# Kernel tuning notes

Hardware: AMD Instinct MI355X
Metric: run time of the kernel (lower is better)

Reference implementation:

```python
import jax, jax.numpy as jnp
import numpy as np

D_MODEL = 1024
NUM_HEADS = 16
D_K = D_MODEL // NUM_HEADS


def setup_inputs() -> dict:
    key = jax.random.key(0)
    ks = jax.random.split(key, 5)
    sd = np.sqrt(2.0 / (D_MODEL + D_MODEL))
    x = jax.random.normal(ks[0], (2, 2048, D_MODEL), dtype=jnp.float32)
    # weights stored as [out_features, in_features] like torch Linear
    w_q = jax.random.normal(ks[1], (D_MODEL, D_MODEL), dtype=jnp.float32) * (sd * sd)
    w_k = jax.random.normal(ks[2], (D_MODEL, D_MODEL), dtype=jnp.float32) * (sd * sd)
    w_v = jax.random.normal(ks[3], (D_MODEL, D_MODEL), dtype=jnp.float32) * (sd * sd)
    w_o = jax.random.normal(ks[4], (D_MODEL, D_MODEL), dtype=jnp.float32) * (sd * sd)
    return {"x": x, "w_q": w_q, "w_k": w_k, "w_v": w_v, "w_o": w_o}


def reference(x, w_q, w_k, w_v, w_o):
    B, S, D = x.shape
    H, Dk = NUM_HEADS, D_K
    # projections: x @ W.T
    q = (x @ w_q.T).reshape(B, S, H, Dk).transpose(0, 2, 1, 3)  # [B,H,S,Dk]
    k = (x @ w_k.T).reshape(B, S, H, Dk).transpose(0, 2, 1, 3)
    v = (x @ w_v.T).reshape(B, S, H, Dk).transpose(0, 2, 1, 3)
    scale = 1.0 / np.sqrt(Dk).astype(np.float32)
    scores = jnp.einsum('bhqd,bhkd->bhqk', q, k) * scale  # [B,H,S,S]
    causal = jnp.tril(jnp.ones((S, S), dtype=bool))
    scores = jnp.where(causal, scores, -jnp.inf)
    weights = jax.nn.softmax(scores, axis=-1)
    attn = jnp.einsum('bhqk,bhkd->bhqd', weights, v)  # [B,H,S,Dk]
    attn = attn.transpose(0, 2, 1, 3).reshape(B, S, D)
    return attn @ w_o.T
```

## Files before the change

kernel.cpp:

```cpp
#include <hip/hip_runtime.h>

typedef __attribute__((ext_vector_type(8))) short short8;
typedef __attribute__((ext_vector_type(4))) float f32x4;
typedef __attribute__((ext_vector_type(16))) float f32x16;
typedef __attribute__((ext_vector_type(2))) unsigned int u32x2;

#define DM 1024
#define SL 2048
#define NH 16
#define DKH 64
#define NB 2

__device__ __forceinline__ unsigned short f2bf(float f) {
    union { float f; unsigned int u; } a; a.f = f;
    unsigned int r = a.u + 0x7FFFu + ((a.u >> 16) & 1u);
    return (unsigned short)(r >> 16);
}

__device__ __forceinline__ void gl_lds16(const void* g, void* l) {
    __builtin_amdgcn_global_load_lds(
        (__attribute__((address_space(1))) void*)(g),
        (__attribute__((address_space(3))) void*)(l), 16, 0, 0);
}

__device__ __forceinline__ unsigned int cvtpk_bf16(float lo, float hi) {
    unsigned int r;
    asm("v_cvt_pk_bf16_f32 %0, %1, %2" : "=v"(r) : "v"(lo), "v"(hi));
    return r;
}

__device__ __forceinline__ void pl32swap(unsigned int &a, unsigned int &b) {
    u32x2 r = __builtin_amdgcn_permlane32_swap(a, b, false, false);
    a = r[0]; b = r[1];
}
__device__ __forceinline__ void pl32swapf(float &a, float &b) {
    unsigned int ua = __float_as_uint(a), ub = __float_as_uint(b);
    pl32swap(ua, ub);
    a = __uint_as_float(ua); b = __uint_as_float(ub);
}

__global__ __launch_bounds__(256) void convert_kernel(
    const float* __restrict__ x,  const float* __restrict__ wq,
    const float* __restrict__ wk, const float* __restrict__ wv,
    const float* __restrict__ wo,
    unsigned short* __restrict__ xb,  unsigned short* __restrict__ wqb,
    unsigned short* __restrict__ wkb, unsigned short* __restrict__ wvb,
    unsigned short* __restrict__ wob)
{
    const int NX = NB * SL * DM;
    const int NW = DM * DM;
    int t4 = (blockIdx.x * 256 + threadIdx.x) * 4;
    const float* src; unsigned short* dst; int off; float scale = 1.0f;
    if (t4 < NX)              { src = x;  dst = xb;  off = t4; }
    else if (t4 < NX + NW)    { src = wq; dst = wqb; off = t4 - NX; scale = 0.125f * 1.44269504088896f; }
    else if (t4 < NX + 2*NW)  { src = wk; dst = wkb; off = t4 - NX - NW; }
    else if (t4 < NX + 3*NW)  { src = wv; dst = wvb; off = t4 - NX - 2*NW; }
    else                      { src = wo; dst = wob; off = t4 - NX - 3*NW; }
    float4 v = *(const float4*)(src + off);
    unsigned long long p =
        (unsigned long long)f2bf(v.x * scale)
      | ((unsigned long long)f2bf(v.y * scale) << 16)
      | ((unsigned long long)f2bf(v.z * scale) << 32)
      | ((unsigned long long)f2bf(v.w * scale) << 48);
    *(unsigned long long*)(dst + off) = p;
}

template<int MODE>
__global__ __launch_bounds__(256) void gemm_bt(
    const unsigned short* __restrict__ A,
    const unsigned short* __restrict__ Bw,
    unsigned short* __restrict__ oq, unsigned short* __restrict__ ok,
    unsigned short* __restrict__ ov, float* __restrict__ of)
{
    __shared__ __align__(16) unsigned short As[128 * 64];
    __shared__ __align__(16) unsigned short Bs[128 * 64];
    const int tid  = threadIdx.x;
    const int lane = tid & 63;
    const int wave = tid >> 6;
    const int wm = (wave >> 1) * 64, wn = (wave & 1) * 64;
    const int bx = blockIdx.x, by = blockIdx.y;
    const int c    = lane & 15;
    const int kg16 = (lane >> 4) * 16;
    const int swz  = (c & 7) << 4;

    f32x4 acc[4][4];
    #pragma unroll
    for (int i = 0; i < 4; i++)
        #pragma unroll
        for (int j = 0; j < 4; j++) acc[i][j] = (f32x4){0.f, 0.f, 0.f, 0.f};

    const char* Ab = (const char*)A  + by * 128 * (DM * 2);
    const char* Bb = (const char*)Bw + bx * 128 * (DM * 2);

    for (int k0 = 0; k0 < DM; k0 += 64) {
        #pragma unroll
        for (int i = 0; i < 4; i++) {
            int o  = i * 4096 + tid * 16;
            int r  = o >> 7;
            int cb = o & 127;
            int src = r * (DM * 2) + k0 * 2 + (cb ^ ((r & 7) << 4));
            gl_lds16(Ab + src, (char*)As + o);
            gl_lds16(Bb + src, (char*)Bs + o);
        }
        __syncthreads();
        #pragma unroll
        for (int kk = 0; kk < 2; kk++) {
            short8 a[4], bfr[4];
            #pragma unroll
            for (int mi = 0; mi < 4; mi++)
                a[mi] = *(const short8*)((const char*)As
                        + (wm + mi * 16 + c) * 128 + ((kk * 64 + kg16) ^ swz));
            #pragma unroll
            for (int ni = 0; ni < 4; ni++)
                bfr[ni] = *(const short8*)((const char*)Bs
                        + (wn + ni * 16 + c) * 128 + ((kk * 64 + kg16) ^ swz));
            #pragma unroll
            for (int mi = 0; mi < 4; mi++)
                #pragma unroll
                for (int ni = 0; ni < 4; ni++)
                    acc[mi][ni] = __builtin_amdgcn_mfma_f32_16x16x32_bf16(
                        a[mi], bfr[ni], acc[mi][ni], 0, 0, 0);
        }
        __syncthreads();
    }

    const int r4 = (lane >> 4) * 4;
    if (MODE == 0) {
        const int mat = (bx * 128) >> 10;
        unsigned short* outb = (mat == 0) ? oq : (mat == 1) ? ok : ov;
        const int nb = bx * 128 - (mat << 10);
        #pragma unroll
        for (int mi = 0; mi < 4; mi++) {
            int m_g = by * 128 + wm + mi * 16 + r4;
            int b_  = m_g >> 11, s_ = m_g & 2047;
            #pragma unroll
            for (int ni = 0; ni < 4; ni++) {
                int n_l = nb + wn + ni * 16 + c;
                int h = n_l >> 6, dk = n_l & 63;
                #pragma unroll
                for (int j = 0; j < 4; j++)
                    outb[((b_ * NH + h) * SL + (s_ + j)) * DKH + dk] = f2bf(acc[mi][ni][j]);
            }
        }
    } else {
        #pragma unroll
        for (int mi = 0; mi < 4; mi++) {
            int m_g = by * 128 + wm + mi * 16 + r4;
            #pragma unroll
            for (int ni = 0; ni < 4; ni++) {
                int n_g = bx * 128 + wn + ni * 16 + c;
                #pragma unroll
                for (int j = 0; j < 4; j++)
                    of[(m_g + j) * DM + n_g] = acc[mi][ni][j];
            }
        }
    }
}

__global__ __launch_bounds__(128) void attn_kernel(
    const unsigned short* __restrict__ Q,
    const unsigned short* __restrict__ K,
    const unsigned short* __restrict__ V,
    unsigned short* __restrict__ O)
{
    __shared__ __align__(16) unsigned short Kl[2][64 * 64];
    __shared__ __align__(16) unsigned short Vt[2][8 * 64 * 8];
    const int tid = threadIdx.x, lane = tid & 63, wave = tid >> 6;
    const int ln31 = lane & 31, hi = lane >> 5;
    const int qt_raw = blockIdx.x >> 5;
    const int bh     = blockIdx.x & 31;
    const int quad = qt_raw >> 3;
    const int qt = (quad == 0) ? qt_raw
                 : (quad == 1) ? (23 - qt_raw)
                 : (quad == 2) ? (qt_raw + 8)
                 :               (47 - qt_raw);
    const int b = bh >> 4, h = bh & 15;
    const int bhi = b * NH + h;
    const unsigned short* Qg = Q + bhi * (SL * DKH);
    const unsigned short* Kg = K + bhi * (SL * DKH);
    const unsigned short* Vg = V + bhi * (SL * DKH);
    const int qw = qt * 64 + wave * 32;
    const int ntiles = qt + 1;
    const int vd0 = (tid & 31) * 2, c0 = tid >> 5;

    short8 qf[4];
    #pragma unroll
    for (int ks = 0; ks < 4; ks++)
        qf[ks] = *(const short8*)&Qg[(qw + ln31) * DKH + ks * 16 + hi * 8];

    f32x16 OT0, OT1;
    #pragma unroll
    for (int r = 0; r < 16; r++) { OT0[r] = 0.f; OT1[r] = 0.f; }
    float mrun = -1e30f, ls = 0.f;

    unsigned int vreg[16];

    #pragma unroll
    for (int i = 0; i < 4; i++) {
        int s = i * 128 + tid;
        int kv = s >> 3;
        int k8 = (s & 7) ^ (kv & 7);
        gl_lds16((const char*)Kg + kv * 128 + k8 * 16, (char*)&Kl[0][0] + s * 16);
    }
    #pragma unroll
    for (int c2 = 0; c2 < 2; c2++)
        #pragma unroll
        for (int i = 0; i < 8; i++)
            vreg[c2 * 8 + i] = *(const unsigned int*)&Vg[((c0 + 4 * c2) * 8 + i) * DKH + vd0];

    for (int t = 0; t < ntiles; ++t) {
        const int buf = t & 1;
        const int kv0 = t * 64;
        #pragma unroll
        for (int c2 = 0; c2 < 2; c2++) {
            int chunk = c0 + 4 * c2;
            short8 sa, sb;
            #pragma unroll
            for (int i = 0; i < 8; i++) {
                unsigned int pr = vreg[c2 * 8 + i];
                sa[i] = (short)(pr & 0xFFFFu);
                sb[i] = (short)(pr >> 16);
            }
            *(short8*)&Vt[buf][(chunk * 64 + vd0) * 8]     = sa;
            *(short8*)&Vt[buf][(chunk * 64 + vd0 + 1) * 8] = sb;
        }
        __syncthreads();

        if (t + 1 < ntiles) {
            const int kv1 = (t + 1) * 64;
            #pragma unroll
            for (int i = 0; i < 4; i++) {
                int s = i * 128 + tid;
                int kv = s >> 3;
                int k8 = (s & 7) ^ (kv & 7);
                gl_lds16((const char*)Kg + (size_t)(kv1 + kv) * 128 + k8 * 16,
                         (char*)&Kl[buf ^ 1][0] + s * 16);
            }
            #pragma unroll
            for (int c2 = 0; c2 < 2; c2++)
                #pragma unroll
                for (int i = 0; i < 8; i++)
                    vreg[c2 * 8 + i] = *(const unsigned int*)&Vg[(size_t)(kv1 + (c0 + 4 * c2) * 8 + i) * DKH + vd0];
        }

        const char* kb = (const char*)&Kl[buf][0];
        const unsigned short* vb = &Vt[buf][0];

        f32x16 S0, S1;
        #pragma unroll
        for (int r = 0; r < 16; r++) { S0[r] = 0.f; S1[r] = 0.f; }
        __builtin_amdgcn_s_setprio(1);
        #pragma unroll
        for (int ks = 0; ks < 4; ks++) {
            int ko = (ks * 32 + hi * 16) ^ ((ln31 & 7) << 4);
            short8 ka0 = *(const short8*)(kb + ln31 * 128 + ko);
            short8 ka1 = *(const short8*)(kb + (32 + ln31) * 128 + ko);
            S0 = __builtin_amdgcn_mfma_f32_32x32x16_bf16(ka0, qf[ks], S0, 0, 0, 0);
            S1 = __builtin_amdgcn_mfma_f32_32x32x16_bf16(ka1, qf[ks], S1, 0, 0, 0);
        }
        __builtin_amdgcn_s_setprio(0);

        if (t == ntiles - 1) {
            const int qrel0 = qw + ln31 - kv0 - 4 * hi;
            const int qrel1 = qrel0 - 32;
            #pragma unroll
            for (int r = 0; r < 16; r++) {
                const int ro = (r & 3) + 8 * (r >> 2);
                if (ro > qrel0) S0[r] = -1e30f;
                if (ro > qrel1) S1[r] = -1e30f;
            }
        }

        float mx = fmaxf(S0[0], S1[0]);
        #pragma unroll
        for (int r = 1; r < 16; r++) mx = fmaxf(mx, fmaxf(S0[r], S1[r]));
        float ma = mx, mb = mx;
        pl32swapf(ma, mb);
        float rm = fmaxf(ma, mb);

        if (__any(rm > mrun + 8.f)) {
            float nm = fmaxf(mrun, rm);
            float corr = __builtin_amdgcn_exp2f(mrun - nm);
            mrun = nm; ls *= corr;
            #pragma unroll
            for (int r = 0; r < 16; r++) { OT0[r] *= corr; OT1[r] *= corr; }
        }

        float psum = 0.f;
        #pragma unroll
        for (int r = 0; r < 16; r++) {
            S0[r] = __builtin_amdgcn_exp2f(S0[r] - mrun); psum += S0[r];
            S1[r] = __builtin_amdgcn_exp2f(S1[r] - mrun); psum += S1[r];
        }
        ls += psum;

        short8 pf[4];
        {
            unsigned int wa, wb, wc, wd;
            wa = cvtpk_bf16(S0[0], S0[1]);   wb = cvtpk_bf16(S0[4], S0[5]);
            pl32swap(wa, wb);
            wc = cvtpk_bf16(S0[2], S0[3]);   wd = cvtpk_bf16(S0[6], S0[7]);
            pl32swap(wc, wd);
            union { unsigned int u[4]; short8 s; } w0 = {{wa, wc, wb, wd}};
            pf[0] = w0.s;

            wa = cvtpk_bf16(S0[8], S0[9]);   wb = cvtpk_bf16(S0[12], S0[13]);
            pl32swap(wa, wb);
            wc = cvtpk_bf16(S0[10], S0[11]); wd = cvtpk_bf16(S0[14], S0[15]);
            pl32swap(wc, wd);
            union { unsigned int u[4]; short8 s; } w1 = {{wa, wc, wb, wd}};
            pf[1] = w1.s;

            wa = cvtpk_bf16(S1[0], S1[1]);   wb = cvtpk_bf16(S1[4], S1[5]);
            pl32swap(wa, wb);
            wc = cvtpk_bf16(S1[2], S1[3]);   wd = cvtpk_bf16(S1[6], S1[7]);
            pl32swap(wc, wd);
            union { unsigned int u[4]; short8 s; } w2 = {{wa, wc, wb, wd}};
            pf[2] = w2.s;

            wa = cvtpk_bf16(S1[8], S1[9]);   wb = cvtpk_bf16(S1[12], S1[13]);
            pl32swap(wa, wb);
            wc = cvtpk_bf16(S1[10], S1[11]); wd = cvtpk_bf16(S1[14], S1[15]);
            pl32swap(wc, wd);
            union { unsigned int u[4]; short8 s; } w3 = {{wa, wc, wb, wd}};
            pf[3] = w3.s;
        }

        __builtin_amdgcn_s_setprio(1);
        #pragma unroll
        for (int ks2 = 0; ks2 < 4; ks2++) {
            int slot = (ks2 * 2 + hi) * 64;
            short8 va0 = *(const short8*)&vb[(slot + ln31) * 8];
            short8 va1 = *(const short8*)&vb[(slot + 32 + ln31) * 8];
            OT0 = __builtin_amdgcn_mfma_f32_32x32x16_bf16(va0, pf[ks2], OT0, 0, 0, 0);
            OT1 = __builtin_amdgcn_mfma_f32_32x32x16_bf16(va1, pf[ks2], OT1, 0, 0, 0);
        }
        __builtin_amdgcn_s_setprio(0);
    }

    float la = ls, lb = ls;
    pl32swapf(la, lb);
    float inv = 1.0f / (la + lb);
    const int qrow = qw + ln31;
    const size_t base = (size_t)(b * SL + qrow) * DM + h * DKH;
    #pragma unroll
    for (int r = 0; r < 16; r++) {
        const int d0 = (r & 3) + 8 * (r >> 2) + 4 * hi;
        O[base + d0]      = f2bf(OT0[r] * inv);
        O[base + 32 + d0] = f2bf(OT1[r] * inv);
    }
}

extern "C" void kernel_launch(void* const* d_in, const int* in_sizes, int n_in,
                              void* d_out, int out_size, void* d_ws, size_t ws_size,
                              hipStream_t stream)
{
    const float* x  = (const float*)d_in[0];
    const float* wq = (const float*)d_in[1];
    const float* wk = (const float*)d_in[2];
    const float* wv = (const float*)d_in[3];
    const float* wo = (const float*)d_in[4];
    char* ws = (char*)d_ws;
    unsigned short* xb  = (unsigned short*)(ws);
    unsigned short* wqb = (unsigned short*)(ws + (8ll  << 20));
    unsigned short* wkb = (unsigned short*)(ws + (10ll << 20));
    unsigned short* wvb = (unsigned short*)(ws + (12ll << 20));
    unsigned short* wob = (unsigned short*)(ws + (14ll << 20));
    unsigned short* Qb  = (unsigned short*)(ws + (16ll << 20));
    unsigned short* Kb  = (unsigned short*)(ws + (24ll << 20));
    unsigned short* Vb  = (unsigned short*)(ws + (32ll << 20));
    unsigned short* Abf = (unsigned short*)(ws + (40ll << 20));
    float* out = (float*)d_out;

    convert_kernel<<<dim3(8192), dim3(256), 0, stream>>>(
        x, wq, wk, wv, wo, xb, wqb, wkb, wvb, wob);

    gemm_bt<0><<<dim3(24, 32), dim3(256), 0, stream>>>(
        xb, wqb, Qb, Kb, Vb, (float*)nullptr);

    attn_kernel<<<dim3(1024), dim3(128), 0, stream>>>(Qb, Kb, Vb, Abf);

    gemm_bt<1><<<dim3(8, 32), dim3(256), 0, stream>>>(
        Abf, wob, nullptr, nullptr, nullptr, out);
}
```

Before: 120.8 us.

## Split long causal query tiles across two KV chunks with a combine pass

Query tiles in the upper half of the sequence are now processed as two blocks. One covers KV tiles 0-15 and the other covers the rest up to the diagonal, so no block walks more than 16 KV tiles. The split blocks write unnormalized bf16 partial outputs plus per-row max and sum to workspace. A new combine kernel merges them with log-sum-exp weighting. This aims to cut the long tail of heavy causal blocks and improve load balance across CUs, at the cost of an extra kernel launch, extra global traffic for the partials, and bf16 rounding of the unnormalized partials.

```diff
diff --git a/kernel.cpp b/kernel.cpp
--- a/kernel.cpp
+++ b/kernel.cpp
@@ -161,26 +161,26 @@
     const unsigned short* __restrict__ Q,
     const unsigned short* __restrict__ K,
     const unsigned short* __restrict__ V,
-    unsigned short* __restrict__ O)
+    unsigned short* __restrict__ O,
+    unsigned short* __restrict__ partO,
+    float* __restrict__ ml)
 {
     __shared__ __align__(16) unsigned short Kl[2][64 * 64];
     __shared__ __align__(16) unsigned short Vt[2][8 * 64 * 8];
     const int tid = threadIdx.x, lane = tid & 63, wave = tid >> 6;
     const int ln31 = lane & 31, hi = lane >> 5;
-    const int qt_raw = blockIdx.x >> 5;
-    const int bh     = blockIdx.x & 31;
-    const int quad = qt_raw >> 3;
-    const int qt = (quad == 0) ? qt_raw
-                 : (quad == 1) ? (23 - qt_raw)
-                 : (quad == 2) ? (qt_raw + 8)
-                 :               (47 - qt_raw);
+    const int item = blockIdx.x >> 5;
+    const int bh   = blockIdx.x & 31;
+    int qt, cch, t0, ntc;
+    if (item < 16)      { qt = 16 + item;              cch = 0; t0 = 0;  ntc = 16; }
+    else if (item < 32) { int j = item - 16; qt = 31 - j; cch = 1; t0 = 16; ntc = 16 - j; }
+    else                { int j = item - 32; qt = 15 - j; cch = 0; t0 = 0;  ntc = 16 - j; }
     const int b = bh >> 4, h = bh & 15;
     const int bhi = b * NH + h;
     const unsigned short* Qg = Q + bhi * (SL * DKH);
     const unsigned short* Kg = K + bhi * (SL * DKH);
     const unsigned short* Vg = V + bhi * (SL * DKH);
     const int qw = qt * 64 + wave * 32;
-    const int ntiles = qt + 1;
     const int vd0 = (tid & 31) * 2, c0 = tid >> 5;
 
     short8 qf[4];
@@ -195,21 +195,26 @@
 
     unsigned int vreg[16];
 
-    #pragma unroll
-    for (int i = 0; i < 4; i++) {
-        int s = i * 128 + tid;
-        int kv = s >> 3;
-        int k8 = (s & 7) ^ (kv & 7);
-        gl_lds16((const char*)Kg + kv * 128 + k8 * 16, (char*)&Kl[0][0] + s * 16);
+    {
+        const size_t kvb = (size_t)t0 * 64;
+        #pragma unroll
+        for (int i = 0; i < 4; i++) {
+            int s = i * 128 + tid;
+            int kv = s >> 3;
+            int k8 = (s & 7) ^ (kv & 7);
+            gl_lds16((const char*)Kg + (kvb + kv) * 128 + k8 * 16,
+                     (char*)&Kl[0][0] + s * 16);
+        }
+        #pragma unroll
+        for (int c2 = 0; c2 < 2; c2++)
+            #pragma unroll
+            for (int i = 0; i < 8; i++)
+                vreg[c2 * 8 + i] = *(const unsigned int*)&Vg[(kvb + (c0 + 4 * c2) * 8 + i) * DKH + vd0];
     }
-    #pragma unroll
-    for (int c2 = 0; c2 < 2; c2++)
-        #pragma unroll
-        for (int i = 0; i < 8; i++)
-            vreg[c2 * 8 + i] = *(const unsigned int*)&Vg[((c0 + 4 * c2) * 8 + i) * DKH + vd0];
-
-    for (int t = 0; t < ntiles; ++t) {
-        const int buf = t & 1;
+
+    for (int tt = 0; tt < ntc; ++tt) {
+        const int t = t0 + tt;
+        const int buf = tt & 1;
         const int kv0 = t * 64;
         #pragma unroll
         for (int c2 = 0; c2 < 2; c2++) {
@@ -226,21 +231,21 @@
         }
         __syncthreads();
 
-        if (t + 1 < ntiles) {
-            const int kv1 = (t + 1) * 64;
+        if (tt + 1 < ntc) {
+            const size_t kv1 = (size_t)(t + 1) * 64;
             #pragma unroll
             for (int i = 0; i < 4; i++) {
                 int s = i * 128 + tid;
                 int kv = s >> 3;
                 int k8 = (s & 7) ^ (kv & 7);
-                gl_lds16((const char*)Kg + (size_t)(kv1 + kv) * 128 + k8 * 16,
+                gl_lds16((const char*)Kg + (kv1 + kv) * 128 + k8 * 16,
                          (char*)&Kl[buf ^ 1][0] + s * 16);
             }
             #pragma unroll
             for (int c2 = 0; c2 < 2; c2++)
                 #pragma unroll
                 for (int i = 0; i < 8; i++)
-                    vreg[c2 * 8 + i] = *(const unsigned int*)&Vg[(size_t)(kv1 + (c0 + 4 * c2) * 8 + i) * DKH + vd0];
+                    vreg[c2 * 8 + i] = *(const unsigned int*)&Vg[(kv1 + (c0 + 4 * c2) * 8 + i) * DKH + vd0];
         }
 
         const char* kb = (const char*)&Kl[buf][0];
@@ -260,7 +265,7 @@
         }
         __builtin_amdgcn_s_setprio(0);
 
-        if (t == ntiles - 1) {
+        if (t == qt) {
             const int qrel0 = qw + ln31 - kv0 - 4 * hi;
             const int qrel1 = qrel0 - 32;
             #pragma unroll
@@ -340,15 +345,64 @@
 
     float la = ls, lb = ls;
     pl32swapf(la, lb);
-    float inv = 1.0f / (la + lb);
-    const int qrow = qw + ln31;
-    const size_t base = (size_t)(b * SL + qrow) * DM + h * DKH;
-    #pragma unroll
-    for (int r = 0; r < 16; r++) {
-        const int d0 = (r & 3) + 8 * (r >> 2) + 4 * hi;
-        O[base + d0]      = f2bf(OT0[r] * inv);
-        O[base + 32 + d0] = f2bf(OT1[r] * inv);
+    const float lrow = la + lb;
+    const int qrow_l = wave * 32 + ln31;
+    if (qt >= 16) {
+        const int rec = (bh * 16 + (qt - 16)) * 2 + cch;
+        unsigned short* po = partO + (size_t)rec * 4096;
+        if (hi == 0) {
+            ml[(rec * 64 + qrow_l) * 2]     = mrun;
+            ml[(rec * 64 + qrow_l) * 2 + 1] = lrow;
+        }
+        #pragma unroll
+        for (int r = 0; r < 16; r++) {
+            const int d0 = (r & 3) + 8 * (r >> 2) + 4 * hi;
+            po[qrow_l * 64 + d0]      = f2bf(OT0[r]);
+            po[qrow_l * 64 + 32 + d0] = f2bf(OT1[r]);
+        }
+    } else {
+        float inv = 1.0f / lrow;
+        const int qrow = qw + ln31;
+        const size_t base = (size_t)(b * SL + qrow) * DM + h * DKH;
+        #pragma unroll
+        for (int r = 0; r < 16; r++) {
+            const int d0 = (r & 3) + 8 * (r >> 2) + 4 * hi;
+            O[base + d0]      = f2bf(OT0[r] * inv);
+            O[base + 32 + d0] = f2bf(OT1[r] * inv);
+        }
     }
+}
+
+__global__ __launch_bounds__(256) void combine_kernel(
+    const unsigned short* __restrict__ partO,
+    const float* __restrict__ ml,
+    unsigned short* __restrict__ O)
+{
+    const int gi = blockIdx.x * 8 + (threadIdx.x >> 5);
+    const int ln = threadIdx.x & 31;
+    const int bh = gi >> 10, rem = gi & 1023;
+    const int qtl = rem >> 6, row = rem & 63;
+    const int qt = 16 + qtl;
+    const int rec0 = (bh * 16 + qtl) * 2;
+    const float m0 = ml[(rec0 * 64 + row) * 2];
+    const float l0 = ml[(rec0 * 64 + row) * 2 + 1];
+    const float m1 = ml[((rec0 + 1) * 64 + row) * 2];
+    const float l1 = ml[((rec0 + 1) * 64 + row) * 2 + 1];
+    const float M  = fmaxf(m0, m1);
+    const float w0 = exp2f(m0 - M), w1 = exp2f(m1 - M);
+    const float inv = 1.0f / (w0 * l0 + w1 * l1);
+    const unsigned int u0 = *(const unsigned int*)&partO[(size_t)rec0 * 4096 + row * 64 + ln * 2];
+    const unsigned int u1 = *(const unsigned int*)&partO[(size_t)(rec0 + 1) * 4096 + row * 64 + ln * 2];
+    const float a0 = __uint_as_float(u0 << 16);
+    const float b0 = __uint_as_float(u0 & 0xFFFF0000u);
+    const float a1 = __uint_as_float(u1 << 16);
+    const float b1 = __uint_as_float(u1 & 0xFFFF0000u);
+    const float oa = (a0 * w0 + a1 * w1) * inv;
+    const float ob = (b0 * w0 + b1 * w1) * inv;
+    const unsigned int pack = (unsigned int)f2bf(oa) | ((unsigned int)f2bf(ob) << 16);
+    const int b = bh >> 4, h = bh & 15;
+    const size_t base = (size_t)(b * SL + qt * 64 + row) * DM + h * DKH;
+    *(unsigned int*)&O[base + ln * 2] = pack;
 }
 
 extern "C" void kernel_launch(void* const* d_in, const int* in_sizes, int n_in,
@@ -370,6 +424,8 @@
     unsigned short* Kb  = (unsigned short*)(ws + (24ll << 20));
     unsigned short* Vb  = (unsigned short*)(ws + (32ll << 20));
     unsigned short* Abf = (unsigned short*)(ws + (40ll << 20));
+    unsigned short* partO = (unsigned short*)(ws);
+    float*          mlbuf = (float*)(ws + (8ll << 20));
     float* out = (float*)d_out;
 
     convert_kernel<<<dim3(8192), dim3(256), 0, stream>>>(
@@ -378,7 +434,8 @@
     gemm_bt<0><<<dim3(24, 32), dim3(256), 0, stream>>>(
         xb, wqb, Qb, Kb, Vb, (float*)nullptr);
 
-    attn_kernel<<<dim3(1024), dim3(128), 0, stream>>>(Qb, Kb, Vb, Abf);
+    attn_kernel<<<dim3(1536), dim3(128), 0, stream>>>(Qb, Kb, Vb, Abf, partO, mlbuf);
+    combine_kernel<<<dim3(4096), dim3(256), 0, stream>>>(partO, mlbuf, Abf);
 
     gemm_bt<1><<<dim3(8, 32), dim3(256), 0, stream>>>(
         Abf, wob, nullptr, nullptr, nullptr, out);
```

After: 111.2 us. 8.0% less time.
